# Performance work log

Hardware: AMD Instinct MI355X
Metric: run time of the kernel (lower is better)

## Reference

```python
import jax, jax.numpy as jnp
import numpy as np

N_EMBED = 1024
N_HEAD = 16
HEAD_DIM = N_EMBED // N_HEAD
N_CONTEXT = 2048
MASKED_BIAS = -10000.0


def setup_inputs() -> dict:
    key = jax.random.key(0)
    k1, k2, k3 = jax.random.split(key, 3)
    hidden_states = jax.random.normal(k1, (4, 2048, N_EMBED), dtype=jnp.float32)
    w_attn = jax.random.normal(k2, (N_EMBED, 3 * N_EMBED), dtype=jnp.float32) * 0.02
    b_attn = jnp.zeros((3 * N_EMBED,), dtype=jnp.float32)
    w_proj = jax.random.normal(k3, (N_EMBED, N_EMBED), dtype=jnp.float32) * 0.02
    b_proj = jnp.zeros((N_EMBED,), dtype=jnp.float32)
    return {"hidden_states": hidden_states, "w_attn": w_attn, "b_attn": b_attn,
            "w_proj": w_proj, "b_proj": b_proj}


def reference(hidden_states, w_attn, b_attn, w_proj, b_proj):
    B, S, E = hidden_states.shape
    # c_attn: Conv1D (x @ W + b)
    qkv = hidden_states @ w_attn + b_attn  # [B,S,3E]
    q, k, v = jnp.split(qkv, 3, axis=-1)
    # split heads -> [B,H,S,D]
    def split_heads(x):
        return x.reshape(B, S, N_HEAD, HEAD_DIM).transpose(0, 2, 1, 3)
    q = split_heads(q)
    k = split_heads(k)  # torch permutes key to [B,H,D,S]; we keep [B,H,S,D] and einsum
    v = split_heads(v)
    # attention scores scaled by sqrt(head_dim) (v.size(-1) == HEAD_DIM)
    w = jnp.einsum('bhqd,bhkd->bhqk', q, k) / jnp.float32(HEAD_DIM) ** 0.5
    causal = jnp.tril(jnp.ones((S, S), dtype=bool))  # bias buffer slice
    w = jnp.where(causal[None, None], w, jnp.asarray(MASKED_BIAS, w.dtype))
    w = jax.nn.softmax(w, axis=-1)  # dropout p=0 -> identity
    out = jnp.einsum('bhqk,bhkd->bhqd', w, v)  # [B,H,S,D]
    # merge heads
    out = out.transpose(0, 2, 1, 3).reshape(B, S, E)
    out = out @ w_proj + b_proj
    # key returned in torch layout [B,H,D,S]
    return out, k.transpose(0, 1, 3, 2), v
```

## Files before the change

kernel.cpp:

```cpp
#include <hip/hip_runtime.h>


typedef __attribute__((ext_vector_type(8))) short bfx8;
typedef __attribute__((ext_vector_type(4))) short bfx4;
typedef __attribute__((ext_vector_type(4))) float fx4;

#define MFMA(a, b, c) __builtin_amdgcn_mfma_f32_16x16x32_bf16(a, b, c, 0, 0, 0)

#define S_CTX 2048
#define NE 1024
#define NH 16
#define HD 64

#define QSCALE 0.18033688011112042f

__device__ __forceinline__ short f2bf(float f) {
  unsigned u = __float_as_uint(f);
  unsigned r = u + 0x7fffu + ((u >> 16) & 1u);
  return (short)(r >> 16);
}

__device__ __forceinline__ void gload16(const void* g, void* l) {
  __builtin_amdgcn_global_load_lds(
      (const __attribute__((address_space(1))) unsigned int*)g,
      (__attribute__((address_space(3))) unsigned int*)l, 16, 0, 0);
}

__global__ __launch_bounds__(256) void convert_bf16_kernel(const float* __restrict__ in,
                                                           short* __restrict__ out) {
  size_t i = (size_t)blockIdx.x * 256 + threadIdx.x;
  fx4 v = *(const fx4*)(in + i * 4);
  bfx4 o;
#pragma unroll
  for (int j = 0; j < 4; ++j) o[j] = f2bf(v[j]);
  *(bfx4*)(out + i * 4) = o;
}

__global__ __launch_bounds__(256) void transpose_conv_kernel(const float* __restrict__ in,
                                                             short* __restrict__ out,
                                                             int R, int C) {
  __shared__ float tile[32][33];
  int tx = threadIdx.x, ty = threadIdx.y;
  int c0 = blockIdx.x * 32, r0 = blockIdx.y * 32;
#pragma unroll
  for (int i = 0; i < 4; ++i)
    tile[ty + i * 8][tx] = in[(size_t)(r0 + ty + i * 8) * C + c0 + tx];
  __syncthreads();
#pragma unroll
  for (int i = 0; i < 4; ++i)
    out[(size_t)(c0 + ty + i * 8) * R + r0 + tx] = f2bf(tile[tx][ty + i * 8]);
}

__device__ __forceinline__ void gemm128_mainloop(const short* __restrict__ A,
                                                 const short* __restrict__ B,
                                                 const int K, const int m0, const int n0,
                                                 short* As, short* Bs, fx4 acc[4][4]) {
  const int t = threadIdx.x;
  const int lane = t & 63, w = t >> 6;
  const int g = lane >> 4, li = lane & 15;
  const int wr = w >> 1, wc = w & 1;
  const int bsw = ((lane & 7) ^ (lane >> 3)) * 8;
  const int rowl = w * 8 + (lane >> 3);

  for (int k0 = 0; k0 < K; k0 += 64) {
#pragma unroll
    for (int i = 0; i < 4; ++i) {
      const int row = i * 32 + rowl;
      gload16(A + (size_t)(m0 + row) * K + k0 + bsw, (char*)As + i * 4096 + w * 1024);
      gload16(B + (size_t)(n0 + row) * K + k0 + bsw, (char*)Bs + i * 4096 + w * 1024);
    }
    __syncthreads();
#pragma unroll
    for (int ks = 0; ks < 2; ++ks) {
      bfx8 af[4], bf[4];
#pragma unroll
      for (int m = 0; m < 4; ++m) {
        const int R = wr * 64 + m * 16 + li;
        af[m] = *(const bfx8*)((const char*)As + R * 128 + (((ks * 4 + g) ^ (li & 7)) << 4));
      }
#pragma unroll
      for (int n = 0; n < 4; ++n) {
        const int R = wc * 64 + n * 16 + li;
        bf[n] = *(const bfx8*)((const char*)Bs + R * 128 + (((ks * 4 + g) ^ (li & 7)) << 4));
      }
#pragma unroll
      for (int m = 0; m < 4; ++m)
#pragma unroll
        for (int n = 0; n < 4; ++n)
          acc[m][n] = MFMA(af[m], bf[n], acc[m][n]);
    }
    __syncthreads();
  }
}

__global__ __launch_bounds__(256) void gemm_qkv_kernel(const short* __restrict__ X,
                                                       const short* __restrict__ WT,
                                                       const float* __restrict__ bias,
                                                       short* __restrict__ qbf,
                                                       short* __restrict__ kbf,
                                                       short* __restrict__ vT,
                                                       float* __restrict__ kT,
                                                       float* __restrict__ vout) {
  __shared__ short As[128 * 64];
  __shared__ short Bs[128 * 64];
  fx4 acc[4][4];
  const fx4 z = {0.f, 0.f, 0.f, 0.f};
#pragma unroll
  for (int m = 0; m < 4; ++m)
#pragma unroll
    for (int n = 0; n < 4; ++n) acc[m][n] = z;
  const int m0 = blockIdx.y * 128, n0 = blockIdx.x * 128;
  gemm128_mainloop(X, WT, 1024, m0, n0, As, Bs, acc);

  const int lane = threadIdx.x & 63, w = threadIdx.x >> 6;
  const int g = lane >> 4, li = lane & 15;
  const int wr = w >> 1, wc = w & 1;
  const int sec = n0 >> 10;
#pragma unroll
  for (int mf = 0; mf < 4; ++mf) {
#pragma unroll
    for (int nf = 0; nf < 4; ++nf) {
      const int mrow = m0 + wr * 64 + mf * 16 + g * 4;
      const int ncol = n0 + wc * 64 + nf * 16 + li;
      const float bv = bias[ncol];
      fx4 vv;
#pragma unroll
      for (int jj = 0; jj < 4; ++jj) vv[jj] = acc[mf][nf][jj] + bv;
      const int b = mrow >> 11, s = mrow & 2047;
      const int e = ncol & 1023, h = e >> 6, d = e & 63;
      const size_t bidx = ((size_t)((b * 16 + h) * 2048 + s)) * 64 + d;
      if (sec == 0) {
#pragma unroll
        for (int jj = 0; jj < 4; ++jj) qbf[bidx + (size_t)jj * 64] = f2bf(vv[jj] * QSCALE);
      } else if (sec == 1) {
#pragma unroll
        for (int jj = 0; jj < 4; ++jj) kbf[bidx + (size_t)jj * 64] = f2bf(vv[jj]);
        const size_t tb = ((size_t)((b * 16 + h) * 64 + d)) * 2048 + s;
        *(fx4*)(kT + tb) = vv;
      } else {
#pragma unroll
        for (int jj = 0; jj < 4; ++jj) vout[bidx + (size_t)jj * 64] = vv[jj];
        const size_t tb = ((size_t)((b * 16 + h) * 64 + d)) * 2048 + s;
        bfx4 pv;
#pragma unroll
        for (int jj = 0; jj < 4; ++jj) pv[jj] = f2bf(vv[jj]);
        *(bfx4*)(vT + tb) = pv;
      }
    }
  }
}

__global__ __launch_bounds__(256) void gemm_proj_kernel(const short* __restrict__ X,
                                                        const short* __restrict__ WT,
                                                        const float* __restrict__ bias,
                                                        float* __restrict__ out) {
  __shared__ short As[128 * 64];
  __shared__ short Bs[128 * 64];
  fx4 acc[4][4];
  const fx4 z = {0.f, 0.f, 0.f, 0.f};
#pragma unroll
  for (int m = 0; m < 4; ++m)
#pragma unroll
    for (int n = 0; n < 4; ++n) acc[m][n] = z;
  const int m0 = blockIdx.y * 128, n0 = blockIdx.x * 128;
  gemm128_mainloop(X, WT, 1024, m0, n0, As, Bs, acc);

  const int lane = threadIdx.x & 63, w = threadIdx.x >> 6;
  const int g = lane >> 4, li = lane & 15;
  const int wr = w >> 1, wc = w & 1;
#pragma unroll
  for (int mf = 0; mf < 4; ++mf) {
#pragma unroll
    for (int nf = 0; nf < 4; ++nf) {
      const int mrow = m0 + wr * 64 + mf * 16 + g * 4;
      const int ncol = n0 + wc * 64 + nf * 16 + li;
      const float bv = bias[ncol];
#pragma unroll
      for (int jj = 0; jj < 4; ++jj)
        out[(size_t)(mrow + jj) * 1024 + ncol] = acc[mf][nf][jj] + bv;
    }
  }
}

#define KSW(base, row, byte) ((char*)(base) + (row) * 128 + ((byte) ^ (((row) & 7) << 4)))

__global__ __launch_bounds__(256, 4) void attn_kernel(const short* __restrict__ Q,
                                                      const short* __restrict__ Kc,
                                                      const short* __restrict__ VT,
                                                      short* __restrict__ O) {
  __shared__ short Ks[2][64 * 64];
  __shared__ short Vs[2][64 * 64];

  const int bh = blockIdx.x & 63;
  const int qchunk = 15 - (blockIdx.x >> 6);
  const int q0 = qchunk * 128;

  const int t = threadIdx.x;
  const int w = t >> 6;
  const int lane = t & 63;
  const int g = lane >> 4, li = lane & 15;

  const size_t hoff = (size_t)bh * (S_CTX * HD);
  const short* Qh = Q + hoff;
  const char* Khc = (const char*)(Kc + hoff);
  const char* Vhc = (const char*)(VT + hoff);

  const int lr = lane >> 3;
  const int bsw = ((lane & 7) ^ lr) * 16;
  const int rb0 = w * 16;

  const int qwr = q0 + w * 32;
  bfx8 qf[2][2];
#pragma unroll
  for (int mf = 0; mf < 2; ++mf) {
    const int qm = qwr + mf * 16;
    qf[mf][0] = *(const bfx8*)(Qh + (size_t)(qm + li) * HD + g * 8);
    qf[mf][1] = *(const bfx8*)(Qh + (size_t)(qm + li) * HD + 32 + g * 8);
  }

  fx4 acc[2][4];
  const fx4 z = {0.f, 0.f, 0.f, 0.f};
#pragma unroll
  for (int mf = 0; mf < 2; ++mf)
#pragma unroll
    for (int dt = 0; dt < 4; ++dt) acc[mf][dt] = z;
  float m_run[2] = {-1e30f, -1e30f};
  float l_run[2] = {0.f, 0.f};

  const int qlim = qwr + 31;
  const int tmax = 2 * qchunk + 1;

#define STAGE_TILE(k0s, buf)                                                        \
  {                                                                                 \
    _Pragma("unroll") for (int i = 0; i < 2; ++i) {                                 \
      const int rb = rb0 + i * 8;                                                   \
      const int row = rb + lr;                                                      \
      gload16(Khc + (size_t)((k0s) + row) * 128 + bsw, (char*)Ks[buf] + rb * 128);  \
      gload16(Vhc + (size_t)row * (S_CTX * 2) + (size_t)(k0s) * 2 + bsw,            \
              (char*)Vs[buf] + rb * 128);                                           \
    }                                                                               \
  }

  STAGE_TILE(0, 0);
  __syncthreads();

  for (int tt = 0; tt <= tmax; ++tt) {
    const int cur = tt & 1;
    const int k0 = tt * 64;
    if (tt < tmax) STAGE_TILE(k0 + 64, cur ^ 1);
    if (k0 <= qlim) {
      fx4 st[2][4];
#pragma unroll
      for (int mf = 0; mf < 2; ++mf)
#pragma unroll
        for (int kt = 0; kt < 4; ++kt) st[mf][kt] = z;
#pragma unroll
      for (int h = 0; h < 2; ++h) {
        bfx8 kfh[4];
#pragma unroll
        for (int kt = 0; kt < 4; ++kt)
          kfh[kt] = *(const bfx8*)KSW(Ks[cur], kt * 16 + li, h * 64 + g * 16);
#pragma unroll
        for (int kt = 0; kt < 4; ++kt) {
          st[0][kt] = MFMA(kfh[kt], qf[0][h], st[0][kt]);
          st[1][kt] = MFMA(kfh[kt], qf[1][h], st[1][kt]);
        }
      }
      bfx8 pA[2][2];
#pragma unroll
      for (int mf = 0; mf < 2; ++mf) {
        const int qm = qwr + mf * 16;
        if (k0 + 63 > qm) {
          const int qg = qm + li;
#pragma unroll
          for (int kt = 0; kt < 4; ++kt)
#pragma unroll
            for (int jj = 0; jj < 4; ++jj)
              if (k0 + kt * 16 + g * 4 + jj > qg) st[mf][kt][jj] = -1e30f;
        }
        float pm = st[mf][0][0];
#pragma unroll
        for (int kt = 0; kt < 4; ++kt)
#pragma unroll
          for (int jj = 0; jj < 4; ++jj) pm = fmaxf(pm, st[mf][kt][jj]);
        if (!__all(pm <= m_run[mf] + 6.0f)) {
          pm = fmaxf(pm, __shfl_xor(pm, 16));
          pm = fmaxf(pm, __shfl_xor(pm, 32));
          const float mn = fmaxf(m_run[mf], pm);
          const float rf = __builtin_amdgcn_exp2f(m_run[mf] - mn);
          l_run[mf] *= rf;
          fx4 rfv;
#pragma unroll
          for (int jj = 0; jj < 4; ++jj) rfv[jj] = __shfl(rf, g * 4 + jj);
#pragma unroll
          for (int dt = 0; dt < 4; ++dt) acc[mf][dt] *= rfv;
          m_run[mf] = mn;
        }
        float ls = 0.f;
#pragma unroll
        for (int kt = 0; kt < 4; ++kt)
#pragma unroll
          for (int jj = 0; jj < 4; ++jj) {
            const float pv = __builtin_amdgcn_exp2f(st[mf][kt][jj] - m_run[mf]);
            ls += pv;
            pA[mf][kt >> 1][(kt & 1) * 4 + jj] = f2bf(pv);
          }
        ls += __shfl_xor(ls, 16);
        ls += __shfl_xor(ls, 32);
        l_run[mf] += ls;
      }
#pragma unroll
      for (int kc = 0; kc < 2; ++kc) {
        bfx8 vfc[4];
#pragma unroll
        for (int dt = 0; dt < 4; ++dt) {
          const int row = dt * 16 + li;
          const bfx4 a = *(const bfx4*)KSW(Vs[cur], row, kc * 64 + g * 8);
          const bfx4 b = *(const bfx4*)KSW(Vs[cur], row, kc * 64 + 32 + g * 8);
          bfx8 vv;
#pragma unroll
          for (int j = 0; j < 4; ++j) {
            vv[j] = a[j];
            vv[j + 4] = b[j];
          }
          vfc[dt] = vv;
        }
#pragma unroll
        for (int dt = 0; dt < 4; ++dt) {
          acc[0][dt] = MFMA(pA[0][kc], vfc[dt], acc[0][dt]);
          acc[1][dt] = MFMA(pA[1][kc], vfc[dt], acc[1][dt]);
        }
      }
    }
    __syncthreads();
  }

  const int b = bh >> 4, h = bh & 15;
#pragma unroll
  for (int mf = 0; mf < 2; ++mf) {
    const int qm = qwr + mf * 16;
    fx4 lv;
#pragma unroll
    for (int jj = 0; jj < 4; ++jj) lv[jj] = 1.0f / __shfl(l_run[mf], g * 4 + jj);
#pragma unroll
    for (int dt = 0; dt < 4; ++dt)
#pragma unroll
      for (int jj = 0; jj < 4; ++jj) {
        const int s = qm + g * 4 + jj;
        O[((size_t)(b * S_CTX + s)) * NE + h * HD + dt * 16 + li] =
            f2bf(acc[mf][dt][jj] * lv[jj]);
      }
  }
}

extern "C" void kernel_launch(void* const* d_in, const int* in_sizes, int n_in,
                              void* d_out, int out_size, void* d_ws, size_t ws_size,
                              hipStream_t stream) {
  const float* hs = (const float*)d_in[0];
  const float* w_attn = (const float*)d_in[1];
  const float* b_attn = (const float*)d_in[2];
  const float* w_proj = (const float*)d_in[3];
  const float* b_proj = (const float*)d_in[4];

  float* out = (float*)d_out;
  float* kT_out = out + 8388608;
  float* v_out = out + 2 * 8388608;

  char* ws = (char*)d_ws;
  short* xbf = (short*)ws;
  short* waT = (short*)(ws + 16777216);
  short* vTb = (short*)(ws + 23068672);
  short* qbf = (short*)(ws + 39845888);
  short* kbf = (short*)(ws + 56623104);
  short* wpT = (short*)(ws + 73400320);

  convert_bf16_kernel<<<8192, 256, 0, stream>>>(hs, xbf);
  transpose_conv_kernel<<<dim3(96, 32), dim3(32, 8), 0, stream>>>(w_attn, waT, 1024, 3072);
  transpose_conv_kernel<<<dim3(32, 32), dim3(32, 8), 0, stream>>>(w_proj, wpT, 1024, 1024);
  gemm_qkv_kernel<<<dim3(24, 64), 256, 0, stream>>>(xbf, waT, b_attn, qbf, kbf, vTb,
                                                    kT_out, v_out);
  attn_kernel<<<1024, 256, 0, stream>>>(qbf, kbf, vTb, xbf );
  gemm_proj_kernel<<<dim3(8, 64), 256, 0, stream>>>(xbf, wpT, b_proj, out);
}
```

Measured before the change: 206.2 us.

## Pair complementary causal query tiles per block for balanced attention work

Each attention block now handles two 16-row query strips per wave, one from chunk c and one from chunk 31-c, so every block iterates over roughly the same number of key tiles and the causal triangle is load balanced. The K/V tile staged in LDS is shared by both strips, and the low strip stops computing after its diagonal tile. Softmax is factored into a macro that uses packed bf16 conversion, and the final normalization uses a hardware reciprocal instead of a division. Per-wave work becomes more branchy, and each block now does roughly uniform work instead of the earlier largest-first ordering.

```diff
diff --git a/kernel.cpp b/kernel.cpp
--- a/kernel.cpp
+++ b/kernel.cpp
@@ -1,4 +1,5 @@
 #include <hip/hip_runtime.h>
+#include <hip/hip_bf16.h>
 
 
 typedef __attribute__((ext_vector_type(8))) short bfx8;
@@ -18,6 +19,15 @@
   unsigned u = __float_as_uint(f);
   unsigned r = u + 0x7fffu + ((u >> 16) & 1u);
   return (short)(r >> 16);
+}
+
+__device__ __forceinline__ unsigned pkbf(float a, float b) {
+  union {
+    __hip_bfloat162 h;
+    unsigned u;
+  } c;
+  c.h = __float22bfloat162_rn(make_float2(a, b));
+  return c.u;
 }
 
 __device__ __forceinline__ void gload16(const void* g, void* l) {
@@ -184,6 +194,51 @@
 
 #define KSW(base, row, byte) ((char*)(base) + (row) * 128 + ((byte) ^ (((row) & 7) << 4)))
 
+#define SOFTMAX_TILE(stv, accv, mrun, lrun, pAv, qm, diag)                    \
+  {                                                                          \
+    if (diag) {                                                              \
+      const int qg = (qm) + li;                                              \
+      _Pragma("unroll") for (int kt = 0; kt < 4; ++kt)                       \
+          _Pragma("unroll") for (int jj = 0; jj < 4; ++jj) if (              \
+              k0 + kt * 16 + g * 4 + jj > qg) stv[kt][jj] = -1e30f;          \
+    }                                                                        \
+    float pm = stv[0][0];                                                    \
+    _Pragma("unroll") for (int kt = 0; kt < 4; ++kt)                         \
+        _Pragma("unroll") for (int jj = 0; jj < 4; ++jj) pm =                \
+            fmaxf(pm, stv[kt][jj]);                                          \
+    if (!__all(pm <= (mrun) + 6.0f)) {                                       \
+      pm = fmaxf(pm, __shfl_xor(pm, 16));                                    \
+      pm = fmaxf(pm, __shfl_xor(pm, 32));                                    \
+      const float mn = fmaxf((mrun), pm);                                    \
+      const float rf = __builtin_amdgcn_exp2f((mrun) - mn);                  \
+      (lrun) *= rf;                                                          \
+      fx4 rfv;                                                               \
+      _Pragma("unroll") for (int jj = 0; jj < 4; ++jj) rfv[jj] =             \
+          __shfl(rf, g * 4 + jj);                                            \
+      _Pragma("unroll") for (int dt = 0; dt < 4; ++dt) accv[dt] *= rfv;      \
+      (mrun) = mn;                                                           \
+    }                                                                        \
+    union {                                                                  \
+      bfx8 v;                                                                \
+      unsigned u[4];                                                         \
+    } pk_[2];                                                                \
+    float ls = 0.f;                                                          \
+    _Pragma("unroll") for (int kt = 0; kt < 4; ++kt) {                       \
+      const float p0 = __builtin_amdgcn_exp2f(stv[kt][0] - (mrun));          \
+      const float p1 = __builtin_amdgcn_exp2f(stv[kt][1] - (mrun));          \
+      const float p2 = __builtin_amdgcn_exp2f(stv[kt][2] - (mrun));          \
+      const float p3 = __builtin_amdgcn_exp2f(stv[kt][3] - (mrun));          \
+      ls += (p0 + p1) + (p2 + p3);                                           \
+      pk_[kt >> 1].u[(kt & 1) * 2 + 0] = pkbf(p0, p1);                       \
+      pk_[kt >> 1].u[(kt & 1) * 2 + 1] = pkbf(p2, p3);                       \
+    }                                                                        \
+    ls += __shfl_xor(ls, 16);                                                \
+    ls += __shfl_xor(ls, 32);                                                \
+    (lrun) += ls;                                                            \
+    pAv[0] = pk_[0].v;                                                       \
+    pAv[1] = pk_[1].v;                                                       \
+  }
+
 __global__ __launch_bounds__(256, 4) void attn_kernel(const short* __restrict__ Q,
                                                       const short* __restrict__ Kc,
                                                       const short* __restrict__ VT,
@@ -192,8 +247,7 @@
   __shared__ short Vs[2][64 * 64];
 
   const int bh = blockIdx.x & 63;
-  const int qchunk = 15 - (blockIdx.x >> 6);
-  const int q0 = qchunk * 128;
+  const int c = blockIdx.x >> 6;
 
   const int t = threadIdx.x;
   const int w = t >> 6;
@@ -209,26 +263,24 @@
   const int bsw = ((lane & 7) ^ lr) * 16;
   const int rb0 = w * 16;
 
-  const int qwr = q0 + w * 32;
-  bfx8 qf[2][2];
-#pragma unroll
-  for (int mf = 0; mf < 2; ++mf) {
-    const int qm = qwr + mf * 16;
-    qf[mf][0] = *(const bfx8*)(Qh + (size_t)(qm + li) * HD + g * 8);
-    qf[mf][1] = *(const bfx8*)(Qh + (size_t)(qm + li) * HD + 32 + g * 8);
-  }
-
-  fx4 acc[2][4];
+  const int qm0 = 64 * c + 16 * w;
+  const int qm1 = 64 * (31 - c) + 16 * w;
+  bfx8 qf0[2], qf1[2];
+  qf0[0] = *(const bfx8*)(Qh + (size_t)(qm0 + li) * HD + g * 8);
+  qf0[1] = *(const bfx8*)(Qh + (size_t)(qm0 + li) * HD + 32 + g * 8);
+  qf1[0] = *(const bfx8*)(Qh + (size_t)(qm1 + li) * HD + g * 8);
+  qf1[1] = *(const bfx8*)(Qh + (size_t)(qm1 + li) * HD + 32 + g * 8);
+
+  fx4 acc0[4], acc1[4];
   const fx4 z = {0.f, 0.f, 0.f, 0.f};
 #pragma unroll
-  for (int mf = 0; mf < 2; ++mf)
-#pragma unroll
-    for (int dt = 0; dt < 4; ++dt) acc[mf][dt] = z;
-  float m_run[2] = {-1e30f, -1e30f};
-  float l_run[2] = {0.f, 0.f};
-
-  const int qlim = qwr + 31;
-  const int tmax = 2 * qchunk + 1;
+  for (int dt = 0; dt < 4; ++dt) {
+    acc0[dt] = z;
+    acc1[dt] = z;
+  }
+  float m0 = -1e30f, l0 = 0.f, m1 = -1e30f, l1 = 0.f;
+
+  const int tmax = 31 - c;
 
 #define STAGE_TILE(k0s, buf)                                                        \
   {                                                                                 \
@@ -248,12 +300,11 @@
     const int cur = tt & 1;
     const int k0 = tt * 64;
     if (tt < tmax) STAGE_TILE(k0 + 64, cur ^ 1);
-    if (k0 <= qlim) {
-      fx4 st[2][4];
-#pragma unroll
-      for (int mf = 0; mf < 2; ++mf)
-#pragma unroll
-        for (int kt = 0; kt < 4; ++kt) st[mf][kt] = z;
+    const bool act0 = (tt <= c);
+
+    bfx8 pA0[2], pA1[2];
+    {
+      fx4 st[4] = {z, z, z, z};
 #pragma unroll
       for (int h = 0; h < 2; ++h) {
         bfx8 kfh[4];
@@ -261,75 +312,44 @@
         for (int kt = 0; kt < 4; ++kt)
           kfh[kt] = *(const bfx8*)KSW(Ks[cur], kt * 16 + li, h * 64 + g * 16);
 #pragma unroll
-        for (int kt = 0; kt < 4; ++kt) {
-          st[0][kt] = MFMA(kfh[kt], qf[0][h], st[0][kt]);
-          st[1][kt] = MFMA(kfh[kt], qf[1][h], st[1][kt]);
+        for (int kt = 0; kt < 4; ++kt) st[kt] = MFMA(kfh[kt], qf1[h], st[kt]);
+      }
+      SOFTMAX_TILE(st, acc1, m1, l1, pA1, qm1, tt == tmax);
+    }
+    if (act0) {
+      fx4 st[4] = {z, z, z, z};
+#pragma unroll
+      for (int h = 0; h < 2; ++h) {
+        bfx8 kfh[4];
+#pragma unroll
+        for (int kt = 0; kt < 4; ++kt)
+          kfh[kt] = *(const bfx8*)KSW(Ks[cur], kt * 16 + li, h * 64 + g * 16);
+#pragma unroll
+        for (int kt = 0; kt < 4; ++kt) st[kt] = MFMA(kfh[kt], qf0[h], st[kt]);
+      }
+      SOFTMAX_TILE(st, acc0, m0, l0, pA0, qm0, tt == c);
+    }
+#pragma unroll
+    for (int kc = 0; kc < 2; ++kc) {
+      bfx8 vfc[4];
+#pragma unroll
+      for (int dt = 0; dt < 4; ++dt) {
+        const int row = dt * 16 + li;
+        const bfx4 a = *(const bfx4*)KSW(Vs[cur], row, kc * 64 + g * 8);
+        const bfx4 b = *(const bfx4*)KSW(Vs[cur], row, kc * 64 + 32 + g * 8);
+        bfx8 vv;
+#pragma unroll
+        for (int j = 0; j < 4; ++j) {
+          vv[j] = a[j];
+          vv[j + 4] = b[j];
         }
-      }
-      bfx8 pA[2][2];
-#pragma unroll
-      for (int mf = 0; mf < 2; ++mf) {
-        const int qm = qwr + mf * 16;
-        if (k0 + 63 > qm) {
-          const int qg = qm + li;
-#pragma unroll
-          for (int kt = 0; kt < 4; ++kt)
-#pragma unroll
-            for (int jj = 0; jj < 4; ++jj)
-              if (k0 + kt * 16 + g * 4 + jj > qg) st[mf][kt][jj] = -1e30f;
-        }
-        float pm = st[mf][0][0];
-#pragma unroll
-        for (int kt = 0; kt < 4; ++kt)
-#pragma unroll
-          for (int jj = 0; jj < 4; ++jj) pm = fmaxf(pm, st[mf][kt][jj]);
-        if (!__all(pm <= m_run[mf] + 6.0f)) {
-          pm = fmaxf(pm, __shfl_xor(pm, 16));
-          pm = fmaxf(pm, __shfl_xor(pm, 32));
-          const float mn = fmaxf(m_run[mf], pm);
-          const float rf = __builtin_amdgcn_exp2f(m_run[mf] - mn);
-          l_run[mf] *= rf;
-          fx4 rfv;
-#pragma unroll
-          for (int jj = 0; jj < 4; ++jj) rfv[jj] = __shfl(rf, g * 4 + jj);
-#pragma unroll
-          for (int dt = 0; dt < 4; ++dt) acc[mf][dt] *= rfv;
-          m_run[mf] = mn;
-        }
-        float ls = 0.f;
-#pragma unroll
-        for (int kt = 0; kt < 4; ++kt)
-#pragma unroll
-          for (int jj = 0; jj < 4; ++jj) {
-            const float pv = __builtin_amdgcn_exp2f(st[mf][kt][jj] - m_run[mf]);
-            ls += pv;
-            pA[mf][kt >> 1][(kt & 1) * 4 + jj] = f2bf(pv);
-          }
-        ls += __shfl_xor(ls, 16);
-        ls += __shfl_xor(ls, 32);
-        l_run[mf] += ls;
-      }
-#pragma unroll
-      for (int kc = 0; kc < 2; ++kc) {
-        bfx8 vfc[4];
-#pragma unroll
-        for (int dt = 0; dt < 4; ++dt) {
-          const int row = dt * 16 + li;
-          const bfx4 a = *(const bfx4*)KSW(Vs[cur], row, kc * 64 + g * 8);
-          const bfx4 b = *(const bfx4*)KSW(Vs[cur], row, kc * 64 + 32 + g * 8);
-          bfx8 vv;
-#pragma unroll
-          for (int j = 0; j < 4; ++j) {
-            vv[j] = a[j];
-            vv[j + 4] = b[j];
-          }
-          vfc[dt] = vv;
-        }
-#pragma unroll
-        for (int dt = 0; dt < 4; ++dt) {
-          acc[0][dt] = MFMA(pA[0][kc], vfc[dt], acc[0][dt]);
-          acc[1][dt] = MFMA(pA[1][kc], vfc[dt], acc[1][dt]);
-        }
+        vfc[dt] = vv;
+      }
+#pragma unroll
+      for (int dt = 0; dt < 4; ++dt) acc1[dt] = MFMA(pA1[kc], vfc[dt], acc1[dt]);
+      if (act0) {
+#pragma unroll
+        for (int dt = 0; dt < 4; ++dt) acc0[dt] = MFMA(pA0[kc], vfc[dt], acc0[dt]);
       }
     }
     __syncthreads();
@@ -338,17 +358,20 @@
   const int b = bh >> 4, h = bh & 15;
 #pragma unroll
   for (int mf = 0; mf < 2; ++mf) {
-    const int qm = qwr + mf * 16;
+    const int qm = mf ? qm1 : qm0;
+    const float lr_ = mf ? l1 : l0;
     fx4 lv;
 #pragma unroll
-    for (int jj = 0; jj < 4; ++jj) lv[jj] = 1.0f / __shfl(l_run[mf], g * 4 + jj);
+    for (int jj = 0; jj < 4; ++jj)
+      lv[jj] = __builtin_amdgcn_rcpf(__shfl(lr_, g * 4 + jj));
 #pragma unroll
     for (int dt = 0; dt < 4; ++dt)
 #pragma unroll
       for (int jj = 0; jj < 4; ++jj) {
         const int s = qm + g * 4 + jj;
+        const fx4 av = mf ? acc1[dt] : acc0[dt];
         O[((size_t)(b * S_CTX + s)) * NE + h * HD + dt * 16 + li] =
-            f2bf(acc[mf][dt][jj] * lv[jj]);
+            f2bf(av[jj] * lv[jj]);
       }
   }
 }
```

New measurement: 183.7 us. -10.9%, faster.
